# Kernel tuning notes

Hardware: AMD Instinct MI355X
Metric: run time of the kernel (lower is better)

Reference implementation:

```python
import jax, jax.numpy as jnp
import numpy as np
import math

MIN_NORM = 1e-15
PROJ_EPS = 4e-3  # float32 boundary eps used by HGCN PoincareBall
C = 1.0          # curvature


def _artanh(x):
    return jnp.arctanh(jnp.clip(x, -1.0 + 1e-7, 1.0 - 1e-7))


def proj(x, c):
    norm = jnp.maximum(jnp.linalg.norm(x, axis=-1, keepdims=True), MIN_NORM)
    maxnorm = (1.0 - PROJ_EPS) / jnp.sqrt(c)
    return jnp.where(norm > maxnorm, x / norm * maxnorm, x)


def lambda_x(x, c):
    x2 = jnp.sum(x * x, axis=-1, keepdims=True)
    return 2.0 / jnp.maximum(1.0 - c * x2, MIN_NORM)


def mobius_add(x, y, c):
    x2 = jnp.sum(x * x, axis=-1, keepdims=True)
    y2 = jnp.sum(y * y, axis=-1, keepdims=True)
    xy = jnp.sum(x * y, axis=-1, keepdims=True)
    num = (1.0 + 2.0 * c * xy + c * y2) * x + (1.0 - c * x2) * y
    denom = 1.0 + 2.0 * c * xy + (c ** 2) * x2 * y2
    return num / jnp.maximum(denom, MIN_NORM)


def logmap0(p, c):
    sqrt_c = jnp.sqrt(c)
    p_norm = jnp.maximum(jnp.linalg.norm(p, axis=-1, keepdims=True), MIN_NORM)
    return _artanh(sqrt_c * p_norm) * p / (p_norm * sqrt_c)


def logmap(p1, p2, c):
    # tangent vector at p1 pointing to p2
    sub = mobius_add(-p1, p2, c)
    sub_norm = jnp.maximum(jnp.linalg.norm(sub, axis=-1, keepdims=True), MIN_NORM)
    lam = lambda_x(p1, c)
    sqrt_c = jnp.sqrt(c)
    return 2.0 / (sqrt_c * lam) * _artanh(sqrt_c * sub_norm) * sub / sub_norm


def expmap(u, p, c):
    # exp map of tangent u at base point p
    sqrt_c = jnp.sqrt(c)
    u_norm = jnp.maximum(jnp.linalg.norm(u, axis=-1, keepdims=True), MIN_NORM)
    second = jnp.tanh(sqrt_c / 2.0 * lambda_x(p, c) * u_norm) * u / (sqrt_c * u_norm)
    return mobius_add(p, second, c)


def setup_inputs() -> dict:
    key = jax.random.key(0)
    k1, k2, k3 = jax.random.split(key, 3)
    N, D = 768, 128
    x = jax.random.normal(k1, (N, D), jnp.float32) * 0.1
    x = proj(x, C)  # valid points on the Poincare ball
    adj = (jax.random.uniform(k2, (N, N), jnp.float32) < 0.04).astype(jnp.float32)
    att_w = jax.random.normal(k3, (2 * D, 1), jnp.float32) * (1.0 / math.sqrt(2 * D))
    att_b = jnp.zeros((1,), jnp.float32)
    return {"x": x, "adj": adj, "att_w": att_w, "att_b": att_b}


def reference(x, adj, att_w, att_b):
    c = C
    D = x.shape[-1]
    x_tangent = logmap0(x, c)                               # [N, D]
    # pairwise logmap: tangent at x_i pointing to x_j -> [N, N, D]
    x_local_tangent = logmap(x[:, None, :], x[None, :, :], c)
    # DenseAtt: sigmoid(Linear([xt_i ; xt_j])) * adj, factorized to avoid [N,N,2D]
    s_left = x_tangent @ att_w[:D, 0]                        # [N]
    s_right = x_tangent @ att_w[D:, 0]                       # [N]
    adj_att = jax.nn.sigmoid(s_left[:, None] + s_right[None, :] + att_b[0]) * adj
    support_t = jnp.einsum('ij,ijd->id', adj_att, x_local_tangent)  # [N, D]
    output = proj(expmap(support_t, x, c), c)
    return output
```

## Files before the change

kernel.cpp:

```cpp
#include <hip/hip_runtime.h>
#include <math.h>

#define NN 768
#define DD 128
#define CAP 192

__device__ __forceinline__ float wave_reduce(float v) {
    #pragma unroll
    for (int o = 32; o > 0; o >>= 1) v += __shfl_down(v, o, 64);
    return v;
}

__global__ void precompute_kernel(const float* __restrict__ x,
                                  const float* __restrict__ att_w,
                                  float* __restrict__ x2a,
                                  float* __restrict__ sL,
                                  float* __restrict__ sR) {
    __shared__ float red[3][2];
    int i = blockIdx.x, t = threadIdx.x;
    float v  = x[i * DD + t];
    float wl = att_w[t];
    float wr = att_w[DD + t];
    float a = wave_reduce(v * v);
    float b = wave_reduce(v * wl);
    float c = wave_reduce(v * wr);
    int wid = t >> 6, lane = t & 63;
    if (lane == 0) { red[0][wid] = a; red[1][wid] = b; red[2][wid] = c; }
    __syncthreads();
    if (t == 0) {
        float x2 = red[0][0] + red[0][1];
        float dl = red[1][0] + red[1][1];
        float dr = red[2][0] + red[2][1];
        float r  = sqrtf(x2);
        float rc = fmaxf(r, 1e-15f);
        float g0 = atanhf(fminf(rc, 1.0f - 1e-7f)) / rc;
        x2a[i] = x2;
        sL[i]  = g0 * dl;
        sR[i]  = g0 * dr;
    }
}

__global__ void pair_kernel(const float* __restrict__ x,
                            const float* __restrict__ adj,
                            const float* __restrict__ x2a,
                            const float* __restrict__ sL,
                            const float* __restrict__ sR,
                            const float* __restrict__ att_b,
                            float* __restrict__ rowA,
                            int* __restrict__ cnt,
                            int* __restrict__ Jlist,
                            float* __restrict__ Blist) {
    __shared__ float xi[DD];
    __shared__ int   list[NN];
    __shared__ float aval[NN];
    __shared__ float dots[NN];
    __shared__ int   counter;
    __shared__ float red[4];

    int i = blockIdx.x, t = threadIdx.x;
    if (t < DD) xi[t] = x[i * DD + t];
    if (t == 0) counter = 0;
    __syncthreads();

    for (int j = t; j < NN; j += 256) {
        float a = adj[i * NN + j];
        if (a != 0.0f) {
            int k = atomicAdd(&counter, 1);
            list[k] = j;
            aval[k] = a;
        }
    }
    __syncthreads();
    int n = counter;

    int wid = t >> 6, lane = t & 63;
    for (int k = wid; k < n; k += 4) {
        int j = list[k];
        float v = xi[lane] * x[j * DD + lane] + xi[lane + 64] * x[j * DD + lane + 64];
        #pragma unroll
        for (int o = 32; o > 0; o >>= 1) v += __shfl_down(v, o, 64);
        if (lane == 0) dots[k] = v;
    }
    __syncthreads();

    float x2i    = x2a[i];
    float beta   = 1.0f - x2i;
    float factor = fmaxf(beta, 1e-15f);
    float sLi    = sL[i];
    float b0     = att_b[0];
    float asum   = 0.0f;
    for (int k = t; k < n; k += 256) {
        int   j   = list[k];
        float dot = dots[k];
        float y2  = x2a[j];
        float z   = sLi + sR[j] + b0;
        float w   = aval[k] / (1.0f + __expf(-z) * 0.0f + expf(-z) * 1.0f - expf(-z) * 0.0f);
        w = aval[k] / (1.0f + expf(-z));
        float alpha  = 1.0f - 2.0f * dot + y2;
        float denom  = 1.0f - 2.0f * dot + x2i * y2;
        float denomc = fmaxf(denom, 1e-15f);
        float sn2 = fmaxf((alpha * alpha * x2i - 2.0f * alpha * beta * dot + beta * beta * y2)
                          / (denomc * denomc), 0.0f);
        float sn = fmaxf(sqrtf(sn2), 1e-15f);
        float g  = atanhf(fminf(sn, 1.0f - 1e-7f)) / sn;
        float common = w * factor * g / denomc;
        asum += -common * alpha;
        if (k < CAP) {
            Blist[i * CAP + k] = common * beta;
            Jlist[i * CAP + k] = j;
        }
    }
    asum = wave_reduce(asum);
    if ((t & 63) == 0) red[t >> 6] = asum;
    __syncthreads();
    if (t == 0) {
        rowA[i] = red[0] + red[1] + red[2] + red[3];
        cnt[i]  = (n < CAP) ? n : CAP;
    }
}

__device__ __forceinline__ float block_reduce_128(float v, float* red) {
    int t = threadIdx.x, wid = t >> 6, lane = t & 63;
    v = wave_reduce(v);
    if (lane == 0) red[wid] = v;
    __syncthreads();
    float r = red[0] + red[1];
    __syncthreads();
    return r;
}

__global__ void agg_kernel(const float* __restrict__ x,
                           const float* __restrict__ x2a,
                           const float* __restrict__ rowA,
                           const int* __restrict__ cnt,
                           const int* __restrict__ Jlist,
                           const float* __restrict__ Blist,
                           float* __restrict__ out) {
    __shared__ float red[2];
    __shared__ int   jj[CAP];
    __shared__ float bb[CAP];
    int i = blockIdx.x, t = threadIdx.x;
    int n = cnt[i];
    for (int k = t; k < n; k += DD) {
        jj[k] = Jlist[i * CAP + k];
        bb[k] = Blist[i * CAP + k];
    }
    __syncthreads();

    float xv  = x[i * DD + t];
    float acc = 0.0f;
    for (int k = 0; k < n; ++k) {
        acc += bb[k] * x[jj[k] * DD + t];
    }
    float u = rowA[i] * xv + acc;

    float un2 = block_reduce_128(u * u, red);
    float xu  = block_reduce_128(xv * u, red);

    float x2i    = x2a[i];
    float lamfac = fmaxf(1.0f - x2i, 1e-15f);
    float un     = fmaxf(sqrtf(un2), 1e-15f);
    float th     = tanhf(un / lamfac);
    float s      = th / un;
    float y2     = s * s * un2;
    float xy     = s * xu;
    float c1     = 1.0f + 2.0f * xy + y2;
    float c2     = 1.0f - x2i;
    float den    = fmaxf(1.0f + 2.0f * xy + x2i * y2, 1e-15f);
    float ov     = (c1 * xv + c2 * s * u) / den;

    float on2 = block_reduce_128(ov * ov, red);
    float on  = fmaxf(sqrtf(on2), 1e-15f);
    const float maxn = 1.0f - 4e-3f;
    if (on > maxn) ov *= maxn / on;

    out[i * DD + t] = ov;
}

extern "C" void kernel_launch(void* const* d_in, const int* in_sizes, int n_in,
                              void* d_out, int out_size, void* d_ws, size_t ws_size,
                              hipStream_t stream) {
    const float* x     = (const float*)d_in[0];
    const float* adj   = (const float*)d_in[1];
    const float* att_w = (const float*)d_in[2];
    const float* att_b = (const float*)d_in[3];
    float* out = (float*)d_out;

    float* ws    = (float*)d_ws;
    float* x2a   = ws;
    float* sL    = ws + NN;
    float* sR    = ws + 2 * NN;
    float* rowA  = ws + 3 * NN;
    int*   cnt   = (int*)(ws + 4 * NN);
    int*   Jlist = (int*)(ws + 5 * NN);
    float* Blist = ws + 5 * NN + NN * CAP;

    precompute_kernel<<<NN, DD, 0, stream>>>(x, att_w, x2a, sL, sR);
    pair_kernel<<<NN, 256, 0, stream>>>(x, adj, x2a, sL, sR, att_b, rowA, cnt, Jlist, Blist);
    agg_kernel<<<NN, DD, 0, stream>>>(x, x2a, rowA, cnt, Jlist, Blist, out);
}
```

Baseline: 74.65 us.

## Fuse precompute, pair and aggregation kernels into one per-row kernel

Measured after the change: 78.47 us. 1.05x slower.

```diff
diff --git a/kernel.cpp b/kernel.cpp
--- a/kernel.cpp
+++ b/kernel.cpp
@@ -3,64 +3,63 @@
 
 #define NN 768
 #define DD 128
-#define CAP 192
 
-__device__ __forceinline__ float wave_reduce(float v) {
+__device__ __forceinline__ double wred_d(double v) {
+    #pragma unroll
+    for (int o = 32; o > 0; o >>= 1) v += __shfl_down(v, o, 64);
+    return v;
+}
+__device__ __forceinline__ float wred_f(float v) {
     #pragma unroll
     for (int o = 32; o > 0; o >>= 1) v += __shfl_down(v, o, 64);
     return v;
 }
 
-__global__ void precompute_kernel(const float* __restrict__ x,
-                                  const float* __restrict__ att_w,
-                                  float* __restrict__ x2a,
-                                  float* __restrict__ sL,
-                                  float* __restrict__ sR) {
-    __shared__ float red[3][2];
-    int i = blockIdx.x, t = threadIdx.x;
-    float v  = x[i * DD + t];
-    float wl = att_w[t];
-    float wr = att_w[DD + t];
-    float a = wave_reduce(v * v);
-    float b = wave_reduce(v * wl);
-    float c = wave_reduce(v * wr);
-    int wid = t >> 6, lane = t & 63;
-    if (lane == 0) { red[0][wid] = a; red[1][wid] = b; red[2][wid] = c; }
-    __syncthreads();
-    if (t == 0) {
-        float x2 = red[0][0] + red[0][1];
-        float dl = red[1][0] + red[1][1];
-        float dr = red[2][0] + red[2][1];
-        float r  = sqrtf(x2);
-        float rc = fmaxf(r, 1e-15f);
-        float g0 = atanhf(fminf(rc, 1.0f - 1e-7f)) / rc;
-        x2a[i] = x2;
-        sL[i]  = g0 * dl;
-        sR[i]  = g0 * dr;
-    }
-}
-
-__global__ void pair_kernel(const float* __restrict__ x,
-                            const float* __restrict__ adj,
-                            const float* __restrict__ x2a,
-                            const float* __restrict__ sL,
-                            const float* __restrict__ sR,
-                            const float* __restrict__ att_b,
-                            float* __restrict__ rowA,
-                            int* __restrict__ cnt,
-                            int* __restrict__ Jlist,
-                            float* __restrict__ Blist) {
+__global__ __launch_bounds__(256) void hypagg_fused(
+        const float* __restrict__ x,
+        const float* __restrict__ adj,
+        const float* __restrict__ att_w,
+        const float* __restrict__ att_b,
+        float* __restrict__ out) {
     __shared__ float xi[DD];
+    __shared__ float wr[DD];
     __shared__ int   list[NN];
     __shared__ float aval[NN];
     __shared__ float dots[NN];
+    __shared__ float y2s[NN];
+    __shared__ float rds[NN];
+    __shared__ float bco[NN];
     __shared__ int   counter;
-    __shared__ float red[4];
+    __shared__ double pre[2][2];
+    __shared__ double s_x2i, s_beta, s_sLi, s_b0;
+    __shared__ double cpart[4];
+    __shared__ double epart[2][3];
 
-    int i = blockIdx.x, t = threadIdx.x;
-    if (t < DD) xi[t] = x[i * DD + t];
+    const int i = blockIdx.x, t = threadIdx.x;
+    const int wid = t >> 6, lane = t & 63;
+
+    float xv = 0.0f;
+    if (t < DD) {
+        xv = x[i * DD + t];
+        xi[t] = xv;
+        wr[t] = att_w[DD + t];
+        double dx2 = wred_d((double)xv * xv);
+        double dwl = wred_d((double)xv * (double)att_w[t]);
+        if (lane == 0) { pre[wid][0] = dx2; pre[wid][1] = dwl; }
+    }
     if (t == 0) counter = 0;
     __syncthreads();
+
+    if (t == 0) {
+        double x2 = pre[0][0] + pre[1][0];
+        double dl = pre[0][1] + pre[1][1];
+        double r  = sqrt(x2);
+        double g0 = atanh(fmin(r, 1.0 - 1e-7)) / fmax(r, 1e-15);
+        s_x2i = x2;
+        s_beta = 1.0 - x2;
+        s_sLi = g0 * dl;
+        s_b0  = (double)att_b[0];
+    }
 
     for (int j = t; j < NN; j += 256) {
         float a = adj[i * NN + j];
@@ -71,110 +70,82 @@
         }
     }
     __syncthreads();
-    int n = counter;
+    const int n = counter;
 
-    int wid = t >> 6, lane = t & 63;
     for (int k = wid; k < n; k += 4) {
-        int j = list[k];
-        float v = xi[lane] * x[j * DD + lane] + xi[lane + 64] * x[j * DD + lane + 64];
-        #pragma unroll
-        for (int o = 32; o > 0; o >>= 1) v += __shfl_down(v, o, 64);
-        if (lane == 0) dots[k] = v;
+        const float* xj = x + (size_t)list[k] * DD;
+        float a0 = xj[lane], a1 = xj[lane + 64];
+        double dd = wred_d((double)xi[lane] * a0 + (double)xi[lane + 64] * a1);
+        double dy = wred_d((double)a0 * a0 + (double)a1 * a1);
+        float  dr = wred_f(wr[lane] * a0 + wr[lane + 64] * a1);
+        if (lane == 0) { dots[k] = (float)dd; y2s[k] = (float)dy; rds[k] = dr; }
     }
     __syncthreads();
 
-    float x2i    = x2a[i];
-    float beta   = 1.0f - x2i;
-    float factor = fmaxf(beta, 1e-15f);
-    float sLi    = sL[i];
-    float b0     = att_b[0];
-    float asum   = 0.0f;
-    for (int k = t; k < n; k += 256) {
-        int   j   = list[k];
-        float dot = dots[k];
-        float y2  = x2a[j];
-        float z   = sLi + sR[j] + b0;
-        float w   = aval[k] / (1.0f + __expf(-z) * 0.0f + expf(-z) * 1.0f - expf(-z) * 0.0f);
-        w = aval[k] / (1.0f + expf(-z));
-        float alpha  = 1.0f - 2.0f * dot + y2;
-        float denom  = 1.0f - 2.0f * dot + x2i * y2;
-        float denomc = fmaxf(denom, 1e-15f);
-        float sn2 = fmaxf((alpha * alpha * x2i - 2.0f * alpha * beta * dot + beta * beta * y2)
-                          / (denomc * denomc), 0.0f);
-        float sn = fmaxf(sqrtf(sn2), 1e-15f);
-        float g  = atanhf(fminf(sn, 1.0f - 1e-7f)) / sn;
-        float common = w * factor * g / denomc;
-        asum += -common * alpha;
-        if (k < CAP) {
-            Blist[i * CAP + k] = common * beta;
-            Jlist[i * CAP + k] = j;
+    double asum = 0.0;
+    {
+        const double x2i = s_x2i, beta = s_beta, sLi = s_sLi, b0 = s_b0;
+        const double factor = fmax(beta, 1e-15);
+        for (int k = t; k < n; k += 256) {
+            double dot = (double)dots[k];
+            double y2  = (double)y2s[k];
+            double ry  = sqrt(y2);
+            double g0j = atanh(fmin(ry, 1.0 - 1e-7)) / fmax(ry, 1e-15);
+            double z   = sLi + g0j * (double)rds[k] + b0;
+            double w   = (double)aval[k] / (1.0 + exp(-z));
+            double alpha  = 1.0 - 2.0 * dot + y2;
+            double denomc = fmax(1.0 - 2.0 * dot + x2i * y2, 1e-15);
+            double sn2 = (alpha * alpha * x2i - 2.0 * alpha * beta * dot + beta * beta * y2)
+                         / (denomc * denomc);
+            double sn  = fmax(sqrt(fmax(sn2, 0.0)), 1e-15);
+            double g   = atanh(fmin(sn, 1.0 - 1e-7)) / sn;
+            double common = w * factor * g / denomc;
+            asum -= common * alpha;
+            bco[k] = (float)(common * beta);
         }
     }
-    asum = wave_reduce(asum);
-    if ((t & 63) == 0) red[t >> 6] = asum;
+    asum = wred_d(asum);
+    if (lane == 0) cpart[wid] = asum;
     __syncthreads();
-    if (t == 0) {
-        rowA[i] = red[0] + red[1] + red[2] + red[3];
-        cnt[i]  = (n < CAP) ? n : CAP;
-    }
-}
 
-__device__ __forceinline__ float block_reduce_128(float v, float* red) {
-    int t = threadIdx.x, wid = t >> 6, lane = t & 63;
-    v = wave_reduce(v);
-    if (lane == 0) red[wid] = v;
-    __syncthreads();
-    float r = red[0] + red[1];
-    __syncthreads();
-    return r;
-}
-
-__global__ void agg_kernel(const float* __restrict__ x,
-                           const float* __restrict__ x2a,
-                           const float* __restrict__ rowA,
-                           const int* __restrict__ cnt,
-                           const int* __restrict__ Jlist,
-                           const float* __restrict__ Blist,
-                           float* __restrict__ out) {
-    __shared__ float red[2];
-    __shared__ int   jj[CAP];
-    __shared__ float bb[CAP];
-    int i = blockIdx.x, t = threadIdx.x;
-    int n = cnt[i];
-    for (int k = t; k < n; k += DD) {
-        jj[k] = Jlist[i * CAP + k];
-        bb[k] = Blist[i * CAP + k];
+    double u = 0.0;
+    if (t < DD) {
+        const double rowA = cpart[0] + cpart[1] + cpart[2] + cpart[3];
+        u = rowA * (double)xv;
+        for (int k = 0; k < n; ++k)
+            u += (double)bco[k] * (double)x[(size_t)list[k] * DD + t];
+        double p_un2 = wred_d(u * u);
+        double p_xu  = wred_d((double)xv * u);
+        if (lane == 0) { epart[wid][0] = p_un2; epart[wid][1] = p_xu; }
     }
     __syncthreads();
 
-    float xv  = x[i * DD + t];
-    float acc = 0.0f;
-    for (int k = 0; k < n; ++k) {
-        acc += bb[k] * x[jj[k] * DD + t];
+    double ov = 0.0;
+    if (t < DD) {
+        double un2 = epart[0][0] + epart[1][0];
+        double xu  = epart[0][1] + epart[1][1];
+        double lamfac = fmax(s_beta, 1e-15);
+        double un = fmax(sqrt(un2), 1e-15);
+        double th = tanh(un / lamfac);
+        double s  = th / un;
+        double y2 = s * s * un2;
+        double xy = s * xu;
+        double c1 = 1.0 + 2.0 * xy + y2;
+        double c2 = 1.0 - s_x2i;
+        double den = fmax(1.0 + 2.0 * xy + s_x2i * y2, 1e-15);
+        ov = (c1 * (double)xv + c2 * s * u) / den;
+        double p_on2 = wred_d(ov * ov);
+        if (lane == 0) epart[wid][2] = p_on2;
     }
-    float u = rowA[i] * xv + acc;
+    __syncthreads();
 
-    float un2 = block_reduce_128(u * u, red);
-    float xu  = block_reduce_128(xv * u, red);
-
-    float x2i    = x2a[i];
-    float lamfac = fmaxf(1.0f - x2i, 1e-15f);
-    float un     = fmaxf(sqrtf(un2), 1e-15f);
-    float th     = tanhf(un / lamfac);
-    float s      = th / un;
-    float y2     = s * s * un2;
-    float xy     = s * xu;
-    float c1     = 1.0f + 2.0f * xy + y2;
-    float c2     = 1.0f - x2i;
-    float den    = fmaxf(1.0f + 2.0f * xy + x2i * y2, 1e-15f);
-    float ov     = (c1 * xv + c2 * s * u) / den;
-
-    float on2 = block_reduce_128(ov * ov, red);
-    float on  = fmaxf(sqrtf(on2), 1e-15f);
-    const float maxn = 1.0f - 4e-3f;
-    if (on > maxn) ov *= maxn / on;
-
-    out[i * DD + t] = ov;
+    if (t < DD) {
+        double on2 = epart[0][2] + epart[1][2];
+        double on  = fmax(sqrt(on2), 1e-15);
+        const double maxn = 1.0 - 4e-3;
+        double scale = (on > maxn) ? (maxn / on) : 1.0;
+        out[i * DD + t] = (float)(ov * scale);
+    }
 }
 
 extern "C" void kernel_launch(void* const* d_in, const int* in_sizes, int n_in,
@@ -185,17 +156,5 @@
     const float* att_w = (const float*)d_in[2];
     const float* att_b = (const float*)d_in[3];
     float* out = (float*)d_out;
-
-    float* ws    = (float*)d_ws;
-    float* x2a   = ws;
-    float* sL    = ws + NN;
-    float* sR    = ws + 2 * NN;
-    float* rowA  = ws + 3 * NN;
-    int*   cnt   = (int*)(ws + 4 * NN);
-    int*   Jlist = (int*)(ws + 5 * NN);
-    float* Blist = ws + 5 * NN + NN * CAP;
-
-    precompute_kernel<<<NN, DD, 0, stream>>>(x, att_w, x2a, sL, sR);
-    pair_kernel<<<NN, 256, 0, stream>>>(x, adj, x2a, sL, sR, att_b, rowA, cnt, Jlist, Blist);
-    agg_kernel<<<NN, DD, 0, stream>>>(x, x2a, rowA, cnt, Jlist, Blist, out);
+    hypagg_fused<<<NN, 256, 0, stream>>>(x, adj, att_w, att_b, out);
 }
```
